# Optimization experiments

Hardware: AMD Instinct MI355X
Metric: run time of the kernel (lower is better)

## Reference

```python
import jax, jax.numpy as jnp
import numpy as np

B, S, E, H, C = 16, 2048, 128, 768, 457


def setup_inputs() -> dict:
    key = jax.random.key(0)
    ks = jax.random.split(key, 8)
    hidden_states = jax.random.normal(ks[0], (B, S, H), dtype=jnp.float32)
    field_labels = jax.random.randint(ks[1], (B, S), 0, C, dtype=jnp.int64) if jax.config.jax_enable_x64 else jax.random.randint(ks[1], (B, S), 0, C, dtype=jnp.int32)
    label_masks = jax.random.randint(ks[2], (B, S), 0, 2, dtype=jnp.int32)
    entities_attr = jax.random.randint(ks[3], (B, E), 0, C, dtype=jnp.int32)
    entities_list = (jax.random.uniform(ks[4], (B, S, E)) < 0.05).astype(jnp.int32)
    entities_len = jnp.maximum(entities_list.sum(axis=1), 1).astype(jnp.int32)  # (B, E)
    entities_mask = jax.random.randint(ks[5], (B, E), 0, 2).astype(bool)
    W = jax.random.normal(ks[6], (C, H), dtype=jnp.float32) * 0.02
    b = jax.random.normal(ks[7], (C,), dtype=jnp.float32) * 0.02
    return {"hidden_states": hidden_states, "field_labels": field_labels,
            "label_masks": label_masks, "entities_attr": entities_attr,
            "entities_list": entities_list, "entities_len": entities_len,
            "entities_mask": entities_mask, "W": W, "b": b}


def reference(hidden_states, field_labels, label_masks, entities_attr,
              entities_list, entities_len, entities_mask, W, b):
    # Entity mean-pool: torch does (B,E,S,H) expand*mul->sum; algebraically a bmm.
    dt = hidden_states.dtype
    ent_hidden = jnp.einsum('bsh,bse->beh', hidden_states, entities_list.astype(dt))
    ent_hidden = ent_hidden / entities_len.astype(dt)[..., None]        # (B,E,H)
    mc_logits = jnp.einsum('beh,ch->bec', ent_hidden, W) + b             # (B,E,C)
    # masked CrossEntropyLoss (mean over selected entities)
    logp = jax.nn.log_softmax(mc_logits, axis=-1)
    nll = -jnp.take_along_axis(logp, entities_attr[..., None].astype(jnp.int32), axis=-1)[..., 0]
    m = entities_mask.astype(dt)
    mask_loss = (nll * m).sum() / m.sum()
    return mask_loss
```

## Files before the change

kernel.cpp:

```cpp
#include <hip/hip_runtime.h>
#include <hip/hip_bf16.h>
#include <cstdint>
#include <cstddef>

constexpr int Bn = 16, Sn = 2048, En = 128, Hn = 768, Cn = 457;
constexpr int NP = 512;
using f32x4  = __attribute__((ext_vector_type(4))) float;
using bf16x8 = __attribute__((ext_vector_type(8))) short;

static __device__ inline unsigned short f2bf(float x) {
  __hip_bfloat16 b = __float2bfloat16(x);
  return *reinterpret_cast<unsigned short*>(&b);
}
static __device__ inline float bflo(unsigned int u) {
  unsigned int v = u << 16;
  return *reinterpret_cast<float*>(&v);
}
static __device__ inline float bfhi(unsigned int u) {
  unsigned int v = u & 0xFFFF0000u;
  return *reinterpret_cast<float*>(&v);
}

__global__ __launch_bounds__(256) void pack_k(
    const int* __restrict__ el, unsigned int* __restrict__ pk2)
{
  const int l = threadIdx.x & 63;
  const int gw = blockIdx.x * 4 + (threadIdx.x >> 6);
  #pragma unroll 8
  for (int j = 0; j < 8; ++j) {
    const int tok = gw * 8 + j;
    const int b = tok >> 11, s = tok & 2047;
    const int v0 = el[(size_t)tok * 128 + l];
    const int v1 = el[(size_t)tok * 128 + 64 + l];
    const unsigned long long b0 = __ballot(v0 != 0);
    const unsigned long long b1 = __ballot(v1 != 0);
    if (l == 0) {
      unsigned int* p = pk2 + (size_t)b * 4 * Sn + s;
      p[0]          = (unsigned int)b0;
      p[Sn]         = (unsigned int)(b0 >> 32);
      p[2 * Sn]     = (unsigned int)b1;
      p[3 * Sn]     = (unsigned int)(b1 >> 32);
    }
  }
}

constexpr int PBN = 64, PBK = 32, PLD = 40;
constexpr int SCH = 4, SLEN = Sn / SCH, PNK = SLEN / PBK;
__global__ __launch_bounds__(512, 6) void pool_k(
    const float* __restrict__ hidden,
    const unsigned int* __restrict__ pk2,
    unsigned short* __restrict__ entp)
{
  const int b = blockIdx.x, n0 = blockIdx.y * PBN, sc = blockIdx.z;
  const int s0 = sc * SLEN;
  const int tid = threadIdx.x, l = tid & 63, wv = tid >> 6;
  const int wm = wv >> 2, wn = wv & 3;

  __shared__ unsigned short Bs[2][PBN][PLD];
  __shared__ unsigned int   PK2[4 * SLEN];

  {
    const int w = tid >> 7, off = (tid & 127) * 4;
    const uint4 v = *reinterpret_cast<const uint4*>(
        pk2 + (size_t)b * 4 * Sn + (size_t)w * Sn + s0 + off);
    *reinterpret_cast<uint4*>(&PK2[w * SLEN + off]) = v;
  }

  const float* hb = hidden + ((size_t)b * Sn + s0) * Hn + n0;

  auto loadh = [&](int kk, float (&f)[4]) {
    const int sb = kk * PBK + wv * 4;
    f[0] = hb[(size_t)(sb + 0) * Hn + l];
    f[1] = hb[(size_t)(sb + 1) * Hn + l];
    f[2] = hb[(size_t)(sb + 2) * Hn + l];
    f[3] = hb[(size_t)(sb + 3) * Hn + l];
  };

  auto stage_b = [&](int bsel, const float (&f)[4]) {
    uint2 dh;
    dh.x = (unsigned int)f2bf(f[0]) | ((unsigned int)f2bf(f[1]) << 16);
    dh.y = (unsigned int)f2bf(f[2]) | ((unsigned int)f2bf(f[3]) << 16);
    *reinterpret_cast<uint2*>(&Bs[bsel][l][wv * 4]) = dh;
  };

  f32x4 acc[4] = {};
  const int rl = l & 15, q = l >> 4, kr = q * 8;

  auto mfma_step = [&](int k, int cur) {
    const int sbase = k * PBK + kr;
    const bf16x8 bfr =
        *reinterpret_cast<const bf16x8*>(&Bs[cur][wn * 16 + rl][kr]);
    #pragma unroll
    for (int mp = 0; mp < 2; ++mp) {
      const int w = wm * 2 + mp;
      const uint4 u0 = *reinterpret_cast<const uint4*>(&PK2[w * SLEN + sbase]);
      const uint4 u1 = *reinterpret_cast<const uint4*>(&PK2[w * SLEN + sbase + 4]);
      #pragma unroll
      for (int mh = 0; mh < 2; ++mh) {
        const int bi = mh * 16 + rl;
        bf16x8 afr;
        unsigned int* ap = reinterpret_cast<unsigned int*>(&afr);
        ap[0] = (((u0.x >> bi) & 1u) ? 0x3F80u : 0u) |
                (((u0.y >> bi) & 1u) ? 0x3F800000u : 0u);
        ap[1] = (((u0.z >> bi) & 1u) ? 0x3F80u : 0u) |
                (((u0.w >> bi) & 1u) ? 0x3F800000u : 0u);
        ap[2] = (((u1.x >> bi) & 1u) ? 0x3F80u : 0u) |
                (((u1.y >> bi) & 1u) ? 0x3F800000u : 0u);
        ap[3] = (((u1.z >> bi) & 1u) ? 0x3F80u : 0u) |
                (((u1.w >> bi) & 1u) ? 0x3F800000u : 0u);
        acc[mp * 2 + mh] = __builtin_amdgcn_mfma_f32_16x16x32_bf16(
            afr, bfr, acc[mp * 2 + mh], 0, 0, 0);
      }
    }
  };

  float pf[3][4];
  loadh(0, pf[0]);
  loadh(1, pf[1]);
  __syncthreads();
  stage_b(0, pf[0]);
  __syncthreads();

  #pragma unroll
  for (int k = 0; k < PNK; ++k) {
    if (k + 2 < PNK) loadh(k + 2, pf[(k + 2) % 3]);
    mfma_step(k, k & 1);
    if (k + 1 < PNK) stage_b((k + 1) & 1, pf[(k + 1) % 3]);
    __syncthreads();
  }

  unsigned short* dst = entp + (size_t)sc * Bn * En * Hn;
  const int rg = q * 4;
  const int col = n0 + wn * 16 + rl;
  #pragma unroll
  for (int mi = 0; mi < 4; ++mi) {
    #pragma unroll
    for (int r = 0; r < 4; ++r) {
      const int e = wm * 64 + mi * 16 + rg + r;
      dst[(size_t)(b * En + e) * Hn + col] = f2bf(acc[mi][r]);
    }
  }
}

__global__ __launch_bounds__(384) void finalize_k(
    const unsigned short* __restrict__ entp, const int* __restrict__ elen,
    unsigned short* __restrict__ entbf)
{
  const int be = blockIdx.x, t = threadIdx.x;
  const float inv = 1.0f / (float)elen[be];
  constexpr size_t PSu = (size_t)Bn * En * Hn / 2;
  const unsigned int* src =
      reinterpret_cast<const unsigned int*>(entp) + (size_t)be * (Hn / 2) + t;
  float lo = 0.f, hi = 0.f;
  #pragma unroll
  for (int p = 0; p < SCH; ++p) {
    const unsigned int u = src[p * PSu];
    lo += bflo(u);
    hi += bfhi(u);
  }
  const unsigned int out = (unsigned int)f2bf(lo * inv) |
                           ((unsigned int)f2bf(hi * inv) << 16);
  reinterpret_cast<unsigned int*>(entbf)[(size_t)be * (Hn / 2) + t] = out;
}

__global__ __launch_bounds__(256) void cast_w_k(
    const float* __restrict__ Wm, unsigned short* __restrict__ wbf)
{
  const int c = blockIdx.x;
  const int tid = threadIdx.x;
  unsigned short* dst = wbf + (size_t)c * Hn;
  if (c < Cn) {
    const float* src = Wm + (size_t)c * Hn;
    #pragma unroll
    for (int j = 0; j < 3; ++j) dst[tid + j * 256] = f2bf(src[tid + j * 256]);
  } else {
    #pragma unroll
    for (int j = 0; j < 3; ++j) dst[tid + j * 256] = 0;
  }
}

constexpr int BM = 128, BN = 64, BK = 32, LDP = BK + 24;
__global__ __launch_bounds__(256) void gemm_k(
    const unsigned short* __restrict__ A,
    const unsigned short* __restrict__ Bm,
    float* __restrict__ Cm)
{
  __shared__ unsigned short As[BM][LDP];
  __shared__ unsigned short Bs[BN][LDP];
  const int bm = blockIdx.x, bn = blockIdx.y;
  const int tid = threadIdx.x, lane = tid & 63, wv = tid >> 6;
  const int wm = wv >> 1, wn = wv & 1;

  f32x4 acc[4][2] = {};

  for (int k0 = 0; k0 < Hn; k0 += BK) {
    #pragma unroll
    for (int i = 0; i < 2; ++i) {
      const int idx = tid + i * 256;
      const int r = idx >> 2, kc = (idx & 3) * 8;
      const unsigned short* src = A + (size_t)(bm * BM + r) * Hn + k0 + kc;
      *reinterpret_cast<ulonglong2*>(&As[r][kc]) =
          *reinterpret_cast<const ulonglong2*>(src);
    }
    {
      const int r = tid >> 2, kc = (tid & 3) * 8;
      const unsigned short* src = Bm + (size_t)(bn * BN + r) * Hn + k0 + kc;
      *reinterpret_cast<ulonglong2*>(&Bs[r][kc]) =
          *reinterpret_cast<const ulonglong2*>(src);
    }
    __syncthreads();

    const int kr = (lane >> 4) * 8, rl = lane & 15;
    bf16x8 af[4], bf[2];
    #pragma unroll
    for (int mi = 0; mi < 4; ++mi)
      af[mi] = *reinterpret_cast<const bf16x8*>(&As[wm * 64 + mi * 16 + rl][kr]);
    #pragma unroll
    for (int ni = 0; ni < 2; ++ni)
      bf[ni] = *reinterpret_cast<const bf16x8*>(&Bs[wn * 32 + ni * 16 + rl][kr]);
    #pragma unroll
    for (int mi = 0; mi < 4; ++mi)
      #pragma unroll
      for (int ni = 0; ni < 2; ++ni)
        acc[mi][ni] = __builtin_amdgcn_mfma_f32_16x16x32_bf16(
            af[mi], bf[ni], acc[mi][ni], 0, 0, 0);
    __syncthreads();
  }

  const int cl = lane & 15, rg = (lane >> 4) * 4;
  #pragma unroll
  for (int mi = 0; mi < 4; ++mi)
    #pragma unroll
    for (int ni = 0; ni < 2; ++ni) {
      const int col = bn * BN + wn * 32 + ni * 16 + cl;
      #pragma unroll
      for (int r = 0; r < 4; ++r) {
        const int row = bm * BM + wm * 64 + mi * 16 + rg + r;
        Cm[(size_t)row * NP + col] = acc[mi][ni][r];
      }
    }
}

__global__ __launch_bounds__(256) void ce_k(
    const float* __restrict__ logits,
    const float* __restrict__ bv,
    const int* __restrict__ attr,
    const unsigned char* __restrict__ emask,
    float* __restrict__ nll)
{
  const int wv = threadIdx.x >> 6, lane = threadIdx.x & 63;
  const int be = blockIdx.x * 4 + wv;
  if (!emask[be]) { if (lane == 0) nll[be] = 0.f; return; }
  const float* row = logits + (size_t)be * NP;

  float mx = -3.4e38f;
  for (int i = lane; i < Cn; i += 64) mx = fmaxf(mx, row[i] + bv[i]);
  #pragma unroll
  for (int o = 32; o; o >>= 1) mx = fmaxf(mx, __shfl_xor(mx, o, 64));
  float sm = 0.f;
  for (int i = lane; i < Cn; i += 64) sm += __expf(row[i] + bv[i] - mx);
  #pragma unroll
  for (int o = 32; o; o >>= 1) sm += __shfl_xor(sm, o, 64);
  if (lane == 0) {
    const int tg = attr[be];
    nll[be] = mx + logf(sm) - (row[tg] + bv[tg]);
  }
}

__global__ __launch_bounds__(256) void reduce_k(
    const float* __restrict__ nll,
    const unsigned char* __restrict__ emask,
    float* __restrict__ out)
{
  const int tid = threadIdx.x;
  float s = 0.f, c = 0.f;
  for (int i = tid; i < Bn * En; i += 256) {
    s += nll[i];
    c += (float)emask[i];
  }
  #pragma unroll
  for (int o = 32; o; o >>= 1) {
    s += __shfl_xor(s, o, 64);
    c += __shfl_xor(c, o, 64);
  }
  __shared__ float ws_[4], wc_[4];
  const int wave = tid >> 6, lane = tid & 63;
  if (lane == 0) { ws_[wave] = s; wc_[wave] = c; }
  __syncthreads();
  if (tid == 0) {
    out[0] = (ws_[0] + ws_[1] + ws_[2] + ws_[3]) /
             (wc_[0] + wc_[1] + wc_[2] + wc_[3]);
  }
}

extern "C" void kernel_launch(void* const* d_in, const int* in_sizes, int n_in,
                              void* d_out, int out_size, void* d_ws, size_t ws_size,
                              hipStream_t stream) {
  const float* hidden        = (const float*)d_in[0];
  const int* attr            = (const int*)d_in[3];
  const int* el              = (const int*)d_in[4];
  const int* elen            = (const int*)d_in[5];
  const unsigned char* emask = (const unsigned char*)d_in[6];
  const float* Wm            = (const float*)d_in[7];
  const float* bv            = (const float*)d_in[8];

  unsigned short* entbf = (unsigned short*)d_ws;
  unsigned short* wbf   = entbf + (size_t)Bn * En * Hn;
  float* logits = (float*)(wbf + (size_t)NP * Hn);
  float* nll    = logits + (size_t)Bn * En * NP;
  unsigned int* pk2buf = (unsigned int*)(nll + Bn * En);
  unsigned short* entp =
      (unsigned short*)(pk2buf + (size_t)Bn * 4 * Sn);

  hipLaunchKernelGGL(pack_k, dim3(1024), dim3(256), 0, stream, el, pk2buf);
  hipLaunchKernelGGL(pool_k, dim3(Bn, Hn / PBN, SCH), dim3(512), 0, stream,
                     hidden, pk2buf, entp);
  hipLaunchKernelGGL(finalize_k, dim3(Bn * En), dim3(384), 0, stream,
                     entp, elen, entbf);
  hipLaunchKernelGGL(cast_w_k, dim3(NP), dim3(256), 0, stream, Wm, wbf);
  hipLaunchKernelGGL(gemm_k, dim3(Bn * En / BM, NP / BN), dim3(256), 0, stream,
                     entbf, wbf, logits);
  hipLaunchKernelGGL(ce_k, dim3(Bn * En / 4), dim3(256), 0, stream,
                     logits, bv, attr, emask, nll);
  hipLaunchKernelGGL(reduce_k, dim3(1), dim3(256), 0, stream,
                     nll, emask, (float*)d_out);
}
```

Measured before the change: 63.49 us.

## Fuse W cast into GEMM, deepen pool prefetch, coalesce pack stores

Three separate changes. The bf16 cast of W now happens inside the GEMM's B-tile load, which removes the cast_w_k launch and its workspace buffer but repeats the cast once per GEMM row-block. The pool kernel prefetches hidden states three tiles ahead instead of two, drops the trailing barrier, and replaces __syncthreads with an lgkmcnt wait plus s_barrier. The pack kernel collects ballot words in shared memory and writes them out as contiguous runs of eight instead of scattered single-lane stores.

```diff
diff --git a/kernel.cpp b/kernel.cpp
--- a/kernel.cpp
+++ b/kernel.cpp
@@ -21,26 +21,37 @@
   return *reinterpret_cast<float*>(&v);
 }
 
+#define LGKM_BAR()                                            \
+  do {                                                        \
+    asm volatile("s_waitcnt lgkmcnt(0)" ::: "memory");        \
+    __builtin_amdgcn_s_barrier();                             \
+    asm volatile("" ::: "memory");                            \
+  } while (0)
+
 __global__ __launch_bounds__(256) void pack_k(
     const int* __restrict__ el, unsigned int* __restrict__ pk2)
 {
-  const int l = threadIdx.x & 63;
-  const int gw = blockIdx.x * 4 + (threadIdx.x >> 6);
-  #pragma unroll 8
+  const int l = threadIdx.x & 63, wv = threadIdx.x >> 6;
+  const int gw = blockIdx.x * 4 + wv;
+  __shared__ unsigned int lbuf[4][4][8];
+
+  #pragma unroll
   for (int j = 0; j < 8; ++j) {
     const int tok = gw * 8 + j;
-    const int b = tok >> 11, s = tok & 2047;
     const int v0 = el[(size_t)tok * 128 + l];
     const int v1 = el[(size_t)tok * 128 + 64 + l];
     const unsigned long long b0 = __ballot(v0 != 0);
     const unsigned long long b1 = __ballot(v1 != 0);
-    if (l == 0) {
-      unsigned int* p = pk2 + (size_t)b * 4 * Sn + s;
-      p[0]          = (unsigned int)b0;
-      p[Sn]         = (unsigned int)(b0 >> 32);
-      p[2 * Sn]     = (unsigned int)b1;
-      p[3 * Sn]     = (unsigned int)(b1 >> 32);
-    }
+    if (l < 4) {
+      const unsigned long long src = (l < 2) ? b0 : b1;
+      lbuf[wv][l][j] = (l & 1) ? (unsigned int)(src >> 32) : (unsigned int)src;
+    }
+  }
+  if (l < 32) {
+    const int w = l >> 3, j = l & 7;
+    const int tok0 = gw * 8;
+    const int b = tok0 >> 11, s = tok0 & 2047;
+    pk2[(size_t)b * 4 * Sn + (size_t)w * Sn + s + j] = lbuf[wv][w][j];
   }
 }
 
@@ -114,19 +125,22 @@
     }
   };
 
-  float pf[3][4];
+  float pf[4][4];
   loadh(0, pf[0]);
   loadh(1, pf[1]);
-  __syncthreads();
+  loadh(2, pf[2]);
+  LGKM_BAR();
   stage_b(0, pf[0]);
-  __syncthreads();
+  LGKM_BAR();
 
   #pragma unroll
   for (int k = 0; k < PNK; ++k) {
-    if (k + 2 < PNK) loadh(k + 2, pf[(k + 2) % 3]);
+    if (k + 3 < PNK) loadh(k + 3, pf[(k + 3) & 3]);
     mfma_step(k, k & 1);
-    if (k + 1 < PNK) stage_b((k + 1) & 1, pf[(k + 1) % 3]);
-    __syncthreads();
+    if (k + 1 < PNK) {
+      stage_b((k + 1) & 1, pf[(k + 1) & 3]);
+      LGKM_BAR();
+    }
   }
 
   unsigned short* dst = entp + (size_t)sc * Bn * En * Hn;
@@ -163,26 +177,10 @@
   reinterpret_cast<unsigned int*>(entbf)[(size_t)be * (Hn / 2) + t] = out;
 }
 
-__global__ __launch_bounds__(256) void cast_w_k(
-    const float* __restrict__ Wm, unsigned short* __restrict__ wbf)
-{
-  const int c = blockIdx.x;
-  const int tid = threadIdx.x;
-  unsigned short* dst = wbf + (size_t)c * Hn;
-  if (c < Cn) {
-    const float* src = Wm + (size_t)c * Hn;
-    #pragma unroll
-    for (int j = 0; j < 3; ++j) dst[tid + j * 256] = f2bf(src[tid + j * 256]);
-  } else {
-    #pragma unroll
-    for (int j = 0; j < 3; ++j) dst[tid + j * 256] = 0;
-  }
-}
-
 constexpr int BM = 128, BN = 64, BK = 32, LDP = BK + 24;
 __global__ __launch_bounds__(256) void gemm_k(
     const unsigned short* __restrict__ A,
-    const unsigned short* __restrict__ Bm,
+    const float* __restrict__ Wm,
     float* __restrict__ Cm)
 {
   __shared__ unsigned short As[BM][LDP];
@@ -204,9 +202,19 @@
     }
     {
       const int r = tid >> 2, kc = (tid & 3) * 8;
-      const unsigned short* src = Bm + (size_t)(bn * BN + r) * Hn + k0 + kc;
-      *reinterpret_cast<ulonglong2*>(&Bs[r][kc]) =
-          *reinterpret_cast<const ulonglong2*>(src);
+      const int grow = bn * BN + r;
+      uint2 d0 = {0u, 0u}, d1 = {0u, 0u};
+      if (grow < Cn) {
+        const float* wp = Wm + (size_t)grow * Hn + k0 + kc;
+        const float4 wa = *reinterpret_cast<const float4*>(wp);
+        const float4 wb = *reinterpret_cast<const float4*>(wp + 4);
+        d0.x = (unsigned int)f2bf(wa.x) | ((unsigned int)f2bf(wa.y) << 16);
+        d0.y = (unsigned int)f2bf(wa.z) | ((unsigned int)f2bf(wa.w) << 16);
+        d1.x = (unsigned int)f2bf(wb.x) | ((unsigned int)f2bf(wb.y) << 16);
+        d1.y = (unsigned int)f2bf(wb.z) | ((unsigned int)f2bf(wb.w) << 16);
+      }
+      *reinterpret_cast<uint2*>(&Bs[r][kc]) = d0;
+      *reinterpret_cast<uint2*>(&Bs[r][kc + 4]) = d1;
     }
     __syncthreads();
 
@@ -305,8 +313,7 @@
   const float* bv            = (const float*)d_in[8];
 
   unsigned short* entbf = (unsigned short*)d_ws;
-  unsigned short* wbf   = entbf + (size_t)Bn * En * Hn;
-  float* logits = (float*)(wbf + (size_t)NP * Hn);
+  float* logits = (float*)(entbf + (size_t)Bn * En * Hn);
   float* nll    = logits + (size_t)Bn * En * NP;
   unsigned int* pk2buf = (unsigned int*)(nll + Bn * En);
   unsigned short* entp =
@@ -317,9 +324,8 @@
                      hidden, pk2buf, entp);
   hipLaunchKernelGGL(finalize_k, dim3(Bn * En), dim3(384), 0, stream,
                      entp, elen, entbf);
-  hipLaunchKernelGGL(cast_w_k, dim3(NP), dim3(256), 0, stream, Wm, wbf);
   hipLaunchKernelGGL(gemm_k, dim3(Bn * En / BM, NP / BN), dim3(256), 0, stream,
-                     entbf, wbf, logits);
+                     entbf, Wm, logits);
   hipLaunchKernelGGL(ce_k, dim3(Bn * En / 4), dim3(256), 0, stream,
                      logits, bv, attr, emask, nll);
   hipLaunchKernelGGL(reduce_k, dim3(1), dim3(256), 0, stream,
```

Measured after the change: 68.75 us. 1.08x slower.
